# Kernel tuning notes

Hardware: AMD Instinct MI355X
Metric: run time of the kernel (lower is better)

The kernel has to match this reference:

```python
import jax, jax.numpy as jnp
import numpy as np

D_MODEL = 1024
NHEAD = 16
HEAD_DIM = D_MODEL // NHEAD
B, S = 8, 1024
NEG = -1e9  # finite stand-in for -inf (same softmax result, grad-safe)


def setup_inputs() -> dict:
    key = jax.random.key(0)
    ks = jax.random.split(key, 12)
    sc = 1.0 / np.sqrt(D_MODEL)
    inp = {
        "q": jax.random.normal(ks[0], (B, S, D_MODEL), jnp.float32),
        "k": jax.random.normal(ks[1], (B, S, D_MODEL), jnp.float32),
        "v": jax.random.normal(ks[2], (B, S, D_MODEL), jnp.float32),
        "padding_mask": jax.random.bernoulli(ks[3], 0.1, (B, S)),
        "causal_mask": jnp.where(jnp.tril(jnp.ones((S, S), bool)), 0.0, NEG).astype(jnp.float32),
        "wq": jax.random.normal(ks[4], (D_MODEL, D_MODEL), jnp.float32) * sc,
        "bq": jax.random.normal(ks[5], (D_MODEL,), jnp.float32) * sc,
        "wk": jax.random.normal(ks[6], (D_MODEL, D_MODEL), jnp.float32) * sc,
        "wv": jax.random.normal(ks[7], (D_MODEL, D_MODEL), jnp.float32) * sc,
        "bv": jax.random.normal(ks[8], (D_MODEL,), jnp.float32) * sc,
        "wo": jax.random.normal(ks[9], (D_MODEL, D_MODEL), jnp.float32) * sc,
        "bo": jax.random.normal(ks[10], (D_MODEL,), jnp.float32) * sc,
    }
    return inp


def reference(q, k, v, padding_mask, causal_mask, wq, bq, wk, wv, bv, wo, bo):
    b = q.shape[0]
    # projections (torch Linear: x @ W.T + b); k_linear has no bias
    qp = q @ wq.T + bq
    kp = k @ wk.T
    vp = v @ wv.T + bv
    # [B, S, H, Dh] -> [B, H, S, Dh]
    qh = qp.reshape(b, -1, NHEAD, HEAD_DIM).transpose(0, 2, 1, 3)
    kh = kp.reshape(b, -1, NHEAD, HEAD_DIM).transpose(0, 2, 1, 3)
    vh = vp.reshape(b, -1, NHEAD, HEAD_DIM).transpose(0, 2, 1, 3)
    scores = jnp.einsum("bhqd,bhkd->bhqk", qh, kh) / np.sqrt(HEAD_DIM).astype(np.float32)
    scores = jnp.where(padding_mask[:, None, None, :], NEG, scores)
    scores = scores + causal_mask[None, None, :, :]
    attn = jax.nn.softmax(scores, axis=-1)
    out = jnp.einsum("bhqk,bhkd->bhqd", attn, vh)
    out = out.transpose(0, 2, 1, 3).reshape(b, -1, D_MODEL)
    return out @ wo.T + bo
```

## Files before the change

### kernel.cpp

```cpp
#include <hip/hip_runtime.h>
#include <hip/hip_bf16.h>
#include <cstdint>
#include <math.h>


typedef __bf16 bf16_t;
typedef __bf16 bf16x8 __attribute__((ext_vector_type(8)));
typedef __bf16 bf16x4 __attribute__((ext_vector_type(4)));
typedef float  f32x4  __attribute__((ext_vector_type(4)));

#define MFMA16(a, b, c) __builtin_amdgcn_mfma_f32_16x16x32_bf16((a), (b), (c), 0, 0, 0)
#define NEGV (-1e9f)

__device__ __forceinline__ void gl_lds16(const void* gp, void* lp) {
  __builtin_amdgcn_global_load_lds(
      (__attribute__((address_space(1))) void*)(gp),
      (__attribute__((address_space(3))) void*)(lp), 16, 0, 0);
}

__device__ __forceinline__ unsigned int pk2(float lo, float hi) {
  unsigned short a = __builtin_bit_cast(unsigned short, (bf16_t)lo);
  unsigned short b = __builtin_bit_cast(unsigned short, (bf16_t)hi);
  return (unsigned int)a | ((unsigned int)b << 16);
}

__device__ __forceinline__ void cvt_body(const float* __restrict__ in,
                                         bf16_t* __restrict__ out, int i, int n8) {
  if (i < n8) {
    const float4* p = reinterpret_cast<const float4*>(in) + (size_t)i * 2;
    float4 a = p[0], b = p[1];
    bf16x8 r = {(bf16_t)a.x, (bf16_t)a.y, (bf16_t)a.z, (bf16_t)a.w,
                (bf16_t)b.x, (bf16_t)b.y, (bf16_t)b.z, (bf16_t)b.w};
    *reinterpret_cast<bf16x8*>(out + (size_t)i * 8) = r;
  }
}

__global__ __launch_bounds__(256) void cvt_qkv(const float* __restrict__ a, const float* __restrict__ b,
                                               const float* __restrict__ c,
                                               bf16_t* __restrict__ oa, bf16_t* __restrict__ ob,
                                               bf16_t* __restrict__ oc, int n8) {
  const float* in = blockIdx.y == 0 ? a : (blockIdx.y == 1 ? b : c);
  bf16_t* out     = blockIdx.y == 0 ? oa : (blockIdx.y == 1 ? ob : oc);
  cvt_body(in, out, blockIdx.x * 256 + threadIdx.x, n8);
}

__global__ __launch_bounds__(256) void cvt_w4(const float* __restrict__ a, const float* __restrict__ b,
                                              const float* __restrict__ c, const float* __restrict__ d,
                                              bf16_t* __restrict__ oa, bf16_t* __restrict__ ob,
                                              bf16_t* __restrict__ oc, bf16_t* __restrict__ od, int n8) {
  const float* in = blockIdx.y == 0 ? a : (blockIdx.y == 1 ? b : (blockIdx.y == 2 ? c : d));
  bf16_t* out     = blockIdx.y == 0 ? oa : (blockIdx.y == 1 ? ob : (blockIdx.y == 2 ? oc : od));
  cvt_body(in, out, blockIdx.x * 256 + threadIdx.x, n8);
}

__device__ __forceinline__ void panel_decode(int r, int& bx, int& by) {
  const int t8 = r >> 3;
  bx = t8 & 7;
  by = ((t8 >> 3) << 3) | (r & 7);
}

__global__ __launch_bounds__(256) void gemm_qkv(const bf16_t* __restrict__ qbf,
                                                const bf16_t* __restrict__ kbf,
                                                const bf16_t* __restrict__ vbf,
                                                const bf16_t* __restrict__ wqb,
                                                const bf16_t* __restrict__ wkb,
                                                const bf16_t* __restrict__ wvb,
                                                const float* __restrict__ bq,
                                                const float* __restrict__ bv,
                                                bf16_t* __restrict__ qp,
                                                bf16_t* __restrict__ kp,
                                                bf16_t* __restrict__ vtw) {
  __shared__ bf16_t smem[4][128 * 32];
  const int z = blockIdx.y;
  const bf16_t* A = z == 0 ? qbf : (z == 1 ? kbf : vbf);
  const bf16_t* W = z == 0 ? wqb : (z == 1 ? wkb : wvb);
  const int t = threadIdx.x;
  const int w = t >> 6, l = t & 63, lr = l & 15, lg = l >> 4;
  int bx, by;
  panel_decode((int)blockIdx.x, bx, by);
  const int m0 = by * 128, n0 = bx * 128;
  const int wm = (w >> 1) * 64, wn = (w & 1) * 64;
  const int K = 1024, N = 1024;

  f32x4 acc[4][4] = {};
  const bf16_t* Ag = A + (size_t)(m0 + (t >> 2)) * K + (t & 3) * 8;
  const bf16_t* Wg = W + (size_t)(n0 + (t >> 2)) * K + (t & 3) * 8;

  auto stage = [&](int buf, int kt) {
    gl_lds16(Ag + kt,                  (char*)(smem[buf])     + t * 16);
    gl_lds16(Ag + kt + (size_t)64 * K, (char*)(smem[buf])     + 4096 + t * 16);
    gl_lds16(Wg + kt,                  (char*)(smem[2 + buf]) + t * 16);
    gl_lds16(Wg + kt + (size_t)64 * K, (char*)(smem[2 + buf]) + 4096 + t * 16);
  };

  stage(0, 0);
  __syncthreads();

  for (int it = 0; it < 32; ++it) {
    const int cur = it & 1;
    if (it < 31) stage(cur ^ 1, (it + 1) * 32);

    const char* AsB = (const char*)(smem[cur]);
    const char* BsB = (const char*)(smem[2 + cur]);
    bf16x8 af[4], bfr[4];
#pragma unroll
    for (int mt = 0; mt < 4; mt++)
      af[mt] = *reinterpret_cast<const bf16x8*>(AsB + ((wm + mt * 16 + lr) * 32 + lg * 8) * 2);
#pragma unroll
    for (int nt = 0; nt < 4; nt++)
      bfr[nt] = *reinterpret_cast<const bf16x8*>(BsB + ((wn + nt * 16 + lr) * 32 + lg * 8) * 2);
#pragma unroll
    for (int mt = 0; mt < 4; mt++)
#pragma unroll
      for (int nt = 0; nt < 4; nt++)
        acc[mt][nt] = MFMA16(af[mt], bfr[nt], acc[mt][nt]);
    __syncthreads();
  }

  if (z != 2) {
    bf16_t* outp = (z == 0) ? qp : kp;
    const float sc = (z == 0) ? 0.125f : 1.0f;
#pragma unroll
    for (int nt = 0; nt < 4; nt++) {
      const int col = n0 + wn + nt * 16 + lr;
      const float bb = (z == 0) ? bq[col] : 0.0f;
#pragma unroll
      for (int mt = 0; mt < 4; mt++)
#pragma unroll
        for (int i = 0; i < 4; i++) {
          const int row = m0 + wm + mt * 16 + lg * 4 + i;
          outp[(size_t)row * N + col] = (bf16_t)((acc[mt][nt][i] + bb) * sc);
        }
    }
  } else {
    char* T = (char*)smem;
#pragma unroll
    for (int nt = 0; nt < 4; nt++) {
      const int col_l = wn + nt * 16 + lr;
      const float bb = bv[n0 + col_l];
#pragma unroll
      for (int mt = 0; mt < 4; mt++)
#pragma unroll
        for (int i = 0; i < 4; i++) {
          const int row_l = wm + mt * 16 + lg * 4 + i;
          *(bf16_t*)(T + col_l * 256 + ((row_l * 2) ^ ((col_l & 7) << 4))) =
              (bf16_t)(acc[mt][nt][i] + bb);
        }
    }
    __syncthreads();
    const int b = m0 >> 10, s0 = m0 & 1023;
    const int c_l = t >> 1, half = t & 1;
    bf16_t* dst = vtw + (size_t)(b * 1024 + n0 + c_l) * 1024 + s0 + half * 64;
    const char* Trow = T + c_l * 256;
    const int sw = c_l & 7;
#pragma unroll
    for (int jj = 0; jj < 8; jj++) {
      const int lc = half * 8 + jj;
      bf16x8 vv = *reinterpret_cast<const bf16x8*>(Trow + ((lc ^ sw) << 4));
      *reinterpret_cast<bf16x8*>(dst + jj * 8) = vv;
    }
  }
}

__global__ __launch_bounds__(256) void gemm_out(const bf16_t* __restrict__ A,
                                                const bf16_t* __restrict__ W,
                                                const float* __restrict__ bias,
                                                float* __restrict__ outp) {
  __shared__ bf16_t smem[4][128 * 32];
  const int t = threadIdx.x;
  const int w = t >> 6, l = t & 63, lr = l & 15, lg = l >> 4;
  int bx, by;
  panel_decode((int)blockIdx.x, bx, by);
  const int m0 = by * 128, n0 = bx * 128;
  const int wm = (w >> 1) * 64, wn = (w & 1) * 64;
  const int K = 1024, N = 1024;

  f32x4 acc[4][4] = {};
  const bf16_t* Ag = A + (size_t)(m0 + (t >> 2)) * K + (t & 3) * 8;
  const bf16_t* Wg = W + (size_t)(n0 + (t >> 2)) * K + (t & 3) * 8;

  auto stage = [&](int buf, int kt) {
    gl_lds16(Ag + kt,                  (char*)(smem[buf])     + t * 16);
    gl_lds16(Ag + kt + (size_t)64 * K, (char*)(smem[buf])     + 4096 + t * 16);
    gl_lds16(Wg + kt,                  (char*)(smem[2 + buf]) + t * 16);
    gl_lds16(Wg + kt + (size_t)64 * K, (char*)(smem[2 + buf]) + 4096 + t * 16);
  };

  stage(0, 0);
  __syncthreads();

  for (int it = 0; it < 32; ++it) {
    const int cur = it & 1;
    if (it < 31) stage(cur ^ 1, (it + 1) * 32);

    const char* AsB = (const char*)(smem[cur]);
    const char* BsB = (const char*)(smem[2 + cur]);
    bf16x8 af[4], bfr[4];
#pragma unroll
    for (int mt = 0; mt < 4; mt++)
      af[mt] = *reinterpret_cast<const bf16x8*>(AsB + ((wm + mt * 16 + lr) * 32 + lg * 8) * 2);
#pragma unroll
    for (int nt = 0; nt < 4; nt++)
      bfr[nt] = *reinterpret_cast<const bf16x8*>(BsB + ((wn + nt * 16 + lr) * 32 + lg * 8) * 2);
#pragma unroll
    for (int mt = 0; mt < 4; mt++)
#pragma unroll
      for (int nt = 0; nt < 4; nt++)
        acc[mt][nt] = MFMA16(af[mt], bfr[nt], acc[mt][nt]);
    __syncthreads();
  }

#pragma unroll
  for (int nt = 0; nt < 4; nt++) {
    const int col = n0 + wn + nt * 16 + lr;
    const float bb = bias[col];
#pragma unroll
    for (int mt = 0; mt < 4; mt++)
#pragma unroll
      for (int i = 0; i < 4; i++) {
        const int row = m0 + wm + mt * 16 + lg * 4 + i;
        outp[(size_t)row * N + col] = acc[mt][nt][i] + bb;
      }
  }
}

__device__ __forceinline__ void pack_bfly(const f32x4 (&s)[4], int lg,
                                          bf16x8& pbv0, bf16x8& pbv1) {
  unsigned int u[4][2], sh[4][2];
#pragma unroll
  for (int nt = 0; nt < 4; nt++) {
    u[nt][0] = pk2(s[nt][0], s[nt][1]);
    u[nt][1] = pk2(s[nt][2], s[nt][3]);
  }
#pragma unroll
  for (int nt = 0; nt < 4; nt++) {
    sh[nt][0] = (unsigned int)__shfl_xor((int)u[nt][0], 16, 64);
    sh[nt][1] = (unsigned int)__shfl_xor((int)u[nt][1], 16, 64);
  }
  const bool ev = (lg & 1) == 0;
  unsigned int Y[8];
  Y[0] = ev ? u[0][0] : sh[1][0];  Y[1] = ev ? u[0][1] : sh[1][1];
  Y[2] = ev ? u[2][0] : sh[3][0];  Y[3] = ev ? u[2][1] : sh[3][1];
  Y[4] = ev ? sh[0][0] : u[1][0];  Y[5] = ev ? sh[0][1] : u[1][1];
  Y[6] = ev ? sh[2][0] : u[3][0];  Y[7] = ev ? sh[2][1] : u[3][1];
  const bool mid = (lg == 1) || (lg == 2);
#pragma unroll
  for (int j = 0; j < 8; j++) {
    const unsigned int z = (unsigned int)__shfl_xor((int)Y[j], 48, 64);
    Y[j] = mid ? z : Y[j];
  }
  union U8 { unsigned int u[4]; bf16x8 v; };
  U8 p0, p1;
  p0.u[0] = Y[0]; p0.u[1] = Y[1]; p0.u[2] = Y[4]; p0.u[3] = Y[5];
  p1.u[0] = Y[2]; p1.u[1] = Y[3]; p1.u[2] = Y[6]; p1.u[3] = Y[7];
  pbv0 = p0.v;
  pbv1 = p1.v;
}

__global__ __launch_bounds__(512, 8) void attn_fused(const bf16_t* __restrict__ qp,
                                                     const bf16_t* __restrict__ kp,
                                                     const bf16_t* __restrict__ vt,
                                                     const int* __restrict__ pad,
                                                     bf16_t* __restrict__ outp) {
  __shared__ bf16_t Ks[2][64 * 64];
  __shared__ bf16_t Vts[2][64 * 64];
  __shared__ int padI[1024];
  __shared__ int sfl[8], sfh[8];
  const int t = threadIdx.x, w = t >> 6, l = t & 63, lr = l & 15, lg = l >> 4;
  const int L = (int)blockIdx.x;
  const int bh = (L & 7) + ((L >> 6) << 3);
  const int j = (L >> 3) & 7;
  const int b = bh >> 4, h = bh & 15;
  const int lo = j, hi = 15 - j;

  const int srow = t >> 3, sc = t & 7;
  const int gc = sc ^ (srow & 7);
  const bf16_t* kgb = kp + (size_t)(b * 1024 + srow) * 1024 + h * 64 + gc * 8;
  const bf16_t* vgb = vt + (size_t)(bh * 64 + srow) * 1024 + gc * 8;

  auto stage = [&](int bufi, int k0s) {
    gl_lds16(kgb + (size_t)k0s * 1024, (char*)(Ks[bufi]) + t * 16);
    gl_lds16(vgb + k0s,                (char*)(Vts[bufi]) + t * 16);
  };

  bool unl = false, unh = false;
  for (int jj = t; jj <= hi * 64; jj += 512) {
    const bool u = (pad[b * 1024 + jj] == 0);
    unh |= u;
    unl |= (u && (jj <= lo * 64));
  }
  const bool al = __any(unl), ah = __any(unh);
  if (l == 0) { sfl[w] = al ? 1 : 0; sfh[w] = ah ? 1 : 0; }

  stage(0, 0);
  if (t < 256) gl_lds16(pad + b * 1024 + t * 4, (char*)padI + t * 16);

  const int mytile = (w < 4) ? hi : lo;
  const int qrow_l = mytile * 64 + (w & 3) * 16 + lr;
  const int base16 = mytile * 64 + (w & 3) * 16;
  const bf16_t* qg = qp + (size_t)(b * 1024 + qrow_l) * 1024 + h * 64 + lg * 8;
  const bf16x8 qa0 = *reinterpret_cast<const bf16x8*>(qg);
  const bf16x8 qa1 = *reinterpret_cast<const bf16x8*>(qg + 32);

  __syncthreads();
  int ul = 0, uh = 0;
#pragma unroll
  for (int i = 0; i < 8; i++) { ul |= sfl[i]; uh |= sfh[i]; }
  const bool mydeg = (w < 4) ? (uh == 0) : (ul == 0);
  const int ktEnd = (ul == 0) ? 16 : (hi + 1);

  f32x4 o[4] = {};
  float m_ = -INFINITY, ld_ = 0.0f;

  for (int kt = 0; kt < ktEnd; ++kt) {
    const int cur = kt & 1;
    if (kt + 1 < ktEnd) {
      stage(cur ^ 1, (kt + 1) * 64);
      asm volatile("s_waitcnt vmcnt(2)" ::: "memory");
    } else {
      asm volatile("s_waitcnt vmcnt(0)" ::: "memory");
    }
    __builtin_amdgcn_s_barrier();

    if (kt <= mytile || mydeg) {
      const char* Kb = (const char*)(Ks[cur]);
      const char* Vb = (const char*)(Vts[cur]);
      const int k0 = kt * 64;

      f32x4 s[4] = {};
#pragma unroll
      for (int nt = 0; nt < 4; nt++) {
        const int row = nt * 16 + lr;
        const int sw = (row & 7) << 4;
        bf16x8 kb0 = *reinterpret_cast<const bf16x8*>(Kb + row * 128 + ((lg * 16) ^ sw));
        bf16x8 kb1 = *reinterpret_cast<const bf16x8*>(Kb + row * 128 + ((lg * 16 + 64) ^ sw));
        s[nt] = MFMA16(kb0, qa0, s[nt]);
        s[nt] = MFMA16(kb1, qa1, s[nt]);
      }

      const bool nc = (k0 + 63 > base16);
#pragma unroll
      for (int nt = 0; nt < 4; nt++) {
        const int kc4 = k0 + nt * 16 + lg * 4;
        const int4 pd = *reinterpret_cast<const int4*>(&padI[kc4]);
        const int pdv[4] = {pd.x, pd.y, pd.z, pd.w};
#pragma unroll
        for (int i = 0; i < 4; i++) {
          float v = s[nt][i];
          if (pdv[i]) v = NEGV;
          if (nc && (kc4 + i > qrow_l)) v += NEGV;
          s[nt][i] = v;
        }
      }

      float mx = s[0][0];
#pragma unroll
      for (int nt = 0; nt < 4; nt++)
#pragma unroll
        for (int i = 0; i < 4; i++) mx = fmaxf(mx, s[nt][i]);
      mx = fmaxf(mx, __shfl_xor(mx, 16, 64));
      mx = fmaxf(mx, __shfl_xor(mx, 32, 64));

      if (!__all(mx <= m_ - 88.0f)) {
        if (!__all(mx <= m_ + 8.0f)) {
          const float mn = fmaxf(m_, mx);
          const float scl = __expf(m_ - mn);
          m_ = mn;
          ld_ *= scl;
#pragma unroll
          for (int nt = 0; nt < 4; nt++) o[nt] *= scl;
        }
        float a = 0.0f;
#pragma unroll
        for (int nt = 0; nt < 4; nt++)
#pragma unroll
          for (int i = 0; i < 4; i++) {
            const float p = __expf(s[nt][i] - m_);
            s[nt][i] = p;
            a += p;
          }
        a += __shfl_xor(a, 16, 64);
        a += __shfl_xor(a, 32, 64);
        ld_ += a;

        bf16x8 pb0, pb1;
        pack_bfly(s, lg, pb0, pb1);

#pragma unroll
        for (int nt = 0; nt < 4; nt++) {
          const int vrow = nt * 16 + lr;
          const int vsw = (vrow & 7) << 4;
          bf16x8 vf0 = *reinterpret_cast<const bf16x8*>(Vb + vrow * 128 + ((lg * 16) ^ vsw));
          bf16x8 vf1 = *reinterpret_cast<const bf16x8*>(Vb + vrow * 128 + ((64 + lg * 16) ^ vsw));
          o[nt] = MFMA16(vf0, pb0, o[nt]);
          o[nt] = MFMA16(vf1, pb1, o[nt]);
        }
      }
    }
    __builtin_amdgcn_s_barrier();
  }

  const float rinv = 1.0f / ld_;
#pragma unroll
  for (int nt = 0; nt < 4; nt++) {
    bf16x4 r = {(bf16_t)(o[nt][0] * rinv), (bf16_t)(o[nt][1] * rinv),
                (bf16_t)(o[nt][2] * rinv), (bf16_t)(o[nt][3] * rinv)};
    *reinterpret_cast<bf16x4*>(outp + (size_t)(b * 1024 + qrow_l) * 1024 + h * 64 + nt * 16 + lg * 4) = r;
  }
}

extern "C" void kernel_launch(void* const* d_in, const int* in_sizes, int n_in,
                              void* d_out, int out_size, void* d_ws, size_t ws_size,
                              hipStream_t stream) {
  const float* q   = (const float*)d_in[0];
  const float* k   = (const float*)d_in[1];
  const float* v   = (const float*)d_in[2];
  const int*   pad = (const int*)d_in[3];
  const float* wq  = (const float*)d_in[5];
  const float* bq  = (const float*)d_in[6];
  const float* wk  = (const float*)d_in[7];
  const float* wv  = (const float*)d_in[8];
  const float* bv  = (const float*)d_in[9];
  const float* wo  = (const float*)d_in[10];
  const float* bo  = (const float*)d_in[11];

  const int M = 8192, N = 1024;
  const int nBig = M * N;
  const int nW   = N * 1024;

  char* ws = (char*)d_ws;
  const size_t MiB = 1024 * 1024;
  bf16_t* qbf = (bf16_t*)(ws + 0 * MiB);
  bf16_t* kbf = (bf16_t*)(ws + 16 * MiB);
  bf16_t* vbf = (bf16_t*)(ws + 32 * MiB);
  bf16_t* qp  = (bf16_t*)(ws + 48 * MiB);
  bf16_t* kp  = (bf16_t*)(ws + 64 * MiB);
  bf16_t* vtw = (bf16_t*)(ws + 80 * MiB);
  bf16_t* wqb = (bf16_t*)(ws + 96 * MiB);
  bf16_t* wkb = (bf16_t*)(ws + 98 * MiB);
  bf16_t* wvb = (bf16_t*)(ws + 100 * MiB);
  bf16_t* wob = (bf16_t*)(ws + 102 * MiB);
  bf16_t* attnO = qbf;

  cvt_qkv<<<dim3(nBig / 2048, 3), 256, 0, stream>>>(q, k, v, qbf, kbf, vbf, nBig / 8);
  cvt_w4 <<<dim3(nW / 2048, 4), 256, 0, stream>>>(wq, wk, wv, wo, wqb, wkb, wvb, wob, nW / 8);

  gemm_qkv<<<dim3(512, 3), 256, 0, stream>>>(qbf, kbf, vbf, wqb, wkb, wvb, bq, bv, qp, kp, vtw);

  attn_fused<<<1024, 512, 0, stream>>>(qp, kp, vtw, pad, attnO);

  gemm_out<<<512, 256, 0, stream>>>(attnO, wob, bo, (float*)d_out);
}
```

Baseline: 189.8 us.

## Fuse fp32-to-bf16 activation conversion into QKV projection GEMM A-tile loads

```diff
diff --git a/kernel.cpp b/kernel.cpp
--- a/kernel.cpp
+++ b/kernel.cpp
@@ -35,15 +35,6 @@
   }
 }
 
-__global__ __launch_bounds__(256) void cvt_qkv(const float* __restrict__ a, const float* __restrict__ b,
-                                               const float* __restrict__ c,
-                                               bf16_t* __restrict__ oa, bf16_t* __restrict__ ob,
-                                               bf16_t* __restrict__ oc, int n8) {
-  const float* in = blockIdx.y == 0 ? a : (blockIdx.y == 1 ? b : c);
-  bf16_t* out     = blockIdx.y == 0 ? oa : (blockIdx.y == 1 ? ob : oc);
-  cvt_body(in, out, blockIdx.x * 256 + threadIdx.x, n8);
-}
-
 __global__ __launch_bounds__(256) void cvt_w4(const float* __restrict__ a, const float* __restrict__ b,
                                               const float* __restrict__ c, const float* __restrict__ d,
                                               bf16_t* __restrict__ oa, bf16_t* __restrict__ ob,
@@ -59,9 +50,9 @@
   by = ((t8 >> 3) << 3) | (r & 7);
 }
 
-__global__ __launch_bounds__(256) void gemm_qkv(const bf16_t* __restrict__ qbf,
-                                                const bf16_t* __restrict__ kbf,
-                                                const bf16_t* __restrict__ vbf,
+__global__ __launch_bounds__(256) void gemm_qkv(const float* __restrict__ qf,
+                                                const float* __restrict__ kf,
+                                                const float* __restrict__ vf,
                                                 const bf16_t* __restrict__ wqb,
                                                 const bf16_t* __restrict__ wkb,
                                                 const bf16_t* __restrict__ wvb,
@@ -72,7 +63,7 @@
                                                 bf16_t* __restrict__ vtw) {
   __shared__ bf16_t smem[4][128 * 32];
   const int z = blockIdx.y;
-  const bf16_t* A = z == 0 ? qbf : (z == 1 ? kbf : vbf);
+  const float*  A = z == 0 ? qf : (z == 1 ? kf : vf);
   const bf16_t* W = z == 0 ? wqb : (z == 1 ? wkb : wvb);
   const int t = threadIdx.x;
   const int w = t >> 6, l = t & 63, lr = l & 15, lg = l >> 4;
@@ -83,23 +74,43 @@
   const int K = 1024, N = 1024;
 
   f32x4 acc[4][4] = {};
-  const bf16_t* Ag = A + (size_t)(m0 + (t >> 2)) * K + (t & 3) * 8;
+
+  const int arow = t >> 1, acol = (t & 1) * 16;
+  const float* Agf = A + (size_t)(m0 + arow) * K + acol;
+  char* adst0 = (char*)(smem[0]) + arow * 64 + (t & 1) * 32;
+  char* adst1 = (char*)(smem[1]) + arow * 64 + (t & 1) * 32;
   const bf16_t* Wg = W + (size_t)(n0 + (t >> 2)) * K + (t & 3) * 8;
 
-  auto stage = [&](int buf, int kt) {
-    gl_lds16(Ag + kt,                  (char*)(smem[buf])     + t * 16);
-    gl_lds16(Ag + kt + (size_t)64 * K, (char*)(smem[buf])     + 4096 + t * 16);
+  float4 a0, a1, a2, a3;
+  auto loadA = [&](int kt) {
+    const float4* p = reinterpret_cast<const float4*>(Agf + kt);
+    a0 = p[0]; a1 = p[1]; a2 = p[2]; a3 = p[3];
+  };
+  auto writeA = [&](int buf) {
+    bf16x8 r0 = {(bf16_t)a0.x, (bf16_t)a0.y, (bf16_t)a0.z, (bf16_t)a0.w,
+                 (bf16_t)a1.x, (bf16_t)a1.y, (bf16_t)a1.z, (bf16_t)a1.w};
+    bf16x8 r1 = {(bf16_t)a2.x, (bf16_t)a2.y, (bf16_t)a2.z, (bf16_t)a2.w,
+                 (bf16_t)a3.x, (bf16_t)a3.y, (bf16_t)a3.z, (bf16_t)a3.w};
+    char* d = buf ? adst1 : adst0;
+    *reinterpret_cast<bf16x8*>(d) = r0;
+    *reinterpret_cast<bf16x8*>(d + 16) = r1;
+  };
+  auto stageB = [&](int buf, int kt) {
     gl_lds16(Wg + kt,                  (char*)(smem[2 + buf]) + t * 16);
     gl_lds16(Wg + kt + (size_t)64 * K, (char*)(smem[2 + buf]) + 4096 + t * 16);
   };
 
-  stage(0, 0);
+  loadA(0);
+  stageB(0, 0);
+  writeA(0);
   __syncthreads();
 
   for (int it = 0; it < 32; ++it) {
     const int cur = it & 1;
-    if (it < 31) stage(cur ^ 1, (it + 1) * 32);
-
+    if (it < 31) {
+      loadA((it + 1) * 32);
+      stageB(cur ^ 1, (it + 1) * 32);
+    }
     const char* AsB = (const char*)(smem[cur]);
     const char* BsB = (const char*)(smem[2 + cur]);
     bf16x8 af[4], bfr[4];
@@ -114,6 +125,7 @@
 #pragma unroll
       for (int nt = 0; nt < 4; nt++)
         acc[mt][nt] = MFMA16(af[mt], bfr[nt], acc[mt][nt]);
+    if (it < 31) writeA(cur ^ 1);
     __syncthreads();
   }
 
@@ -424,15 +436,11 @@
   const float* wo  = (const float*)d_in[10];
   const float* bo  = (const float*)d_in[11];
 
-  const int M = 8192, N = 1024;
-  const int nBig = M * N;
-  const int nW   = N * 1024;
+  const int nW = 1024 * 1024;
 
   char* ws = (char*)d_ws;
   const size_t MiB = 1024 * 1024;
-  bf16_t* qbf = (bf16_t*)(ws + 0 * MiB);
-  bf16_t* kbf = (bf16_t*)(ws + 16 * MiB);
-  bf16_t* vbf = (bf16_t*)(ws + 32 * MiB);
+  bf16_t* attnO = (bf16_t*)(ws + 0 * MiB);
   bf16_t* qp  = (bf16_t*)(ws + 48 * MiB);
   bf16_t* kp  = (bf16_t*)(ws + 64 * MiB);
   bf16_t* vtw = (bf16_t*)(ws + 80 * MiB);
@@ -440,12 +448,10 @@
   bf16_t* wkb = (bf16_t*)(ws + 98 * MiB);
   bf16_t* wvb = (bf16_t*)(ws + 100 * MiB);
   bf16_t* wob = (bf16_t*)(ws + 102 * MiB);
-  bf16_t* attnO = qbf;
-
-  cvt_qkv<<<dim3(nBig / 2048, 3), 256, 0, stream>>>(q, k, v, qbf, kbf, vbf, nBig / 8);
-  cvt_w4 <<<dim3(nW / 2048, 4), 256, 0, stream>>>(wq, wk, wv, wo, wqb, wkb, wvb, wob, nW / 8);
-
-  gemm_qkv<<<dim3(512, 3), 256, 0, stream>>>(qbf, kbf, vbf, wqb, wkb, wvb, bq, bv, qp, kp, vtw);
+
+  cvt_w4<<<dim3(nW / 2048, 4), 256, 0, stream>>>(wq, wk, wv, wo, wqb, wkb, wvb, wob, nW / 8);
+
+  gemm_qkv<<<dim3(512, 3), 256, 0, stream>>>(q, k, v, wqb, wkb, wvb, bq, bv, qp, kp, vtw);
 
   attn_fused<<<1024, 512, 0, stream>>>(qp, kp, vtw, pad, attnO);
 
```

After: 194.4 us. 1.02x slower.

## Triple-buffer GEMM LDS staging with swizzled layout and merge conversion kernels

Applied to the files above, without the earlier changes.

```diff
diff --git a/kernel.cpp b/kernel.cpp
--- a/kernel.cpp
+++ b/kernel.cpp
@@ -25,32 +25,34 @@
 }
 
 __device__ __forceinline__ void cvt_body(const float* __restrict__ in,
-                                         bf16_t* __restrict__ out, int i, int n8) {
-  if (i < n8) {
-    const float4* p = reinterpret_cast<const float4*>(in) + (size_t)i * 2;
-    float4 a = p[0], b = p[1];
-    bf16x8 r = {(bf16_t)a.x, (bf16_t)a.y, (bf16_t)a.z, (bf16_t)a.w,
-                (bf16_t)b.x, (bf16_t)b.y, (bf16_t)b.z, (bf16_t)b.w};
-    *reinterpret_cast<bf16x8*>(out + (size_t)i * 8) = r;
-  }
-}
-
-__global__ __launch_bounds__(256) void cvt_qkv(const float* __restrict__ a, const float* __restrict__ b,
-                                               const float* __restrict__ c,
-                                               bf16_t* __restrict__ oa, bf16_t* __restrict__ ob,
-                                               bf16_t* __restrict__ oc, int n8) {
-  const float* in = blockIdx.y == 0 ? a : (blockIdx.y == 1 ? b : c);
-  bf16_t* out     = blockIdx.y == 0 ? oa : (blockIdx.y == 1 ? ob : oc);
-  cvt_body(in, out, blockIdx.x * 256 + threadIdx.x, n8);
-}
-
-__global__ __launch_bounds__(256) void cvt_w4(const float* __restrict__ a, const float* __restrict__ b,
-                                              const float* __restrict__ c, const float* __restrict__ d,
-                                              bf16_t* __restrict__ oa, bf16_t* __restrict__ ob,
-                                              bf16_t* __restrict__ oc, bf16_t* __restrict__ od, int n8) {
-  const float* in = blockIdx.y == 0 ? a : (blockIdx.y == 1 ? b : (blockIdx.y == 2 ? c : d));
-  bf16_t* out     = blockIdx.y == 0 ? oa : (blockIdx.y == 1 ? ob : (blockIdx.y == 2 ? oc : od));
-  cvt_body(in, out, blockIdx.x * 256 + threadIdx.x, n8);
+                                         bf16_t* __restrict__ out, int i) {
+  const float4* p = reinterpret_cast<const float4*>(in) + (size_t)i * 2;
+  float4 a = p[0], b = p[1];
+  bf16x8 r = {(bf16_t)a.x, (bf16_t)a.y, (bf16_t)a.z, (bf16_t)a.w,
+              (bf16_t)b.x, (bf16_t)b.y, (bf16_t)b.z, (bf16_t)b.w};
+  *reinterpret_cast<bf16x8*>(out + (size_t)i * 8) = r;
+}
+
+__global__ __launch_bounds__(256) void cvt_all(
+    const float* __restrict__ q, const float* __restrict__ k, const float* __restrict__ v,
+    const float* __restrict__ wq, const float* __restrict__ wk,
+    const float* __restrict__ wv, const float* __restrict__ wo,
+    bf16_t* __restrict__ oq, bf16_t* __restrict__ ok, bf16_t* __restrict__ ov,
+    bf16_t* __restrict__ owq, bf16_t* __restrict__ owk,
+    bf16_t* __restrict__ owv, bf16_t* __restrict__ owo) {
+  const int bid = (int)blockIdx.x;
+  if (bid < 12288) {
+    const int s = bid >> 12;
+    const int i = (bid & 4095) * 256 + (int)threadIdx.x;
+    cvt_body(s == 0 ? q : (s == 1 ? k : v),
+             s == 0 ? oq : (s == 1 ? ok : ov), i);
+  } else {
+    const int r = bid - 12288;
+    const int s = r >> 9;
+    const int i = (r & 511) * 256 + (int)threadIdx.x;
+    cvt_body(s == 0 ? wq : (s == 1 ? wk : (s == 2 ? wv : wo)),
+             s == 0 ? owq : (s == 1 ? owk : (s == 2 ? owv : owo)), i);
+  }
 }
 
 __device__ __forceinline__ void panel_decode(int r, int& bx, int& by) {
@@ -70,7 +72,7 @@
                                                 bf16_t* __restrict__ qp,
                                                 bf16_t* __restrict__ kp,
                                                 bf16_t* __restrict__ vtw) {
-  __shared__ bf16_t smem[4][128 * 32];
+  __shared__ bf16_t smem[6][128 * 32];
   const int z = blockIdx.y;
   const bf16_t* A = z == 0 ? qbf : (z == 1 ? kbf : vbf);
   const bf16_t* W = z == 0 ? wqb : (z == 1 ? wkb : wvb);
@@ -83,38 +85,42 @@
   const int K = 1024, N = 1024;
 
   f32x4 acc[4][4] = {};
-  const bf16_t* Ag = A + (size_t)(m0 + (t >> 2)) * K + (t & 3) * 8;
-  const bf16_t* Wg = W + (size_t)(n0 + (t >> 2)) * K + (t & 3) * 8;
-
-  auto stage = [&](int buf, int kt) {
+  const int swsrc = ((t & 3) ^ ((t >> 3) & 3)) * 8;
+  const bf16_t* Ag = A + (size_t)(m0 + (t >> 2)) * K + swsrc;
+  const bf16_t* Wg = W + (size_t)(n0 + (t >> 2)) * K + swsrc;
+
+  auto stage = [&](int buf, int tile) {
+    const int kt = tile * 32;
     gl_lds16(Ag + kt,                  (char*)(smem[buf])     + t * 16);
     gl_lds16(Ag + kt + (size_t)64 * K, (char*)(smem[buf])     + 4096 + t * 16);
-    gl_lds16(Wg + kt,                  (char*)(smem[2 + buf]) + t * 16);
-    gl_lds16(Wg + kt + (size_t)64 * K, (char*)(smem[2 + buf]) + 4096 + t * 16);
+    gl_lds16(Wg + kt,                  (char*)(smem[3 + buf]) + t * 16);
+    gl_lds16(Wg + kt + (size_t)64 * K, (char*)(smem[3 + buf]) + 4096 + t * 16);
   };
 
   stage(0, 0);
-  __syncthreads();
-
+  stage(1, 1);
+
+  const int cofs = ((lg ^ ((lr >> 1) & 3)) << 4);
   for (int it = 0; it < 32; ++it) {
-    const int cur = it & 1;
-    if (it < 31) stage(cur ^ 1, (it + 1) * 32);
-
-    const char* AsB = (const char*)(smem[cur]);
-    const char* BsB = (const char*)(smem[2 + cur]);
+    if (it < 31) asm volatile("s_waitcnt vmcnt(4)" ::: "memory");
+    else         asm volatile("s_waitcnt vmcnt(0)" ::: "memory");
+    __builtin_amdgcn_s_barrier();
+    if (it + 2 < 32) stage((it + 2) % 3, it + 2);
+
+    const char* AsB = (const char*)(smem[it % 3]);
+    const char* BsB = (const char*)(smem[3 + it % 3]);
     bf16x8 af[4], bfr[4];
 #pragma unroll
     for (int mt = 0; mt < 4; mt++)
-      af[mt] = *reinterpret_cast<const bf16x8*>(AsB + ((wm + mt * 16 + lr) * 32 + lg * 8) * 2);
+      af[mt] = *reinterpret_cast<const bf16x8*>(AsB + (wm + mt * 16 + lr) * 64 + cofs);
 #pragma unroll
     for (int nt = 0; nt < 4; nt++)
-      bfr[nt] = *reinterpret_cast<const bf16x8*>(BsB + ((wn + nt * 16 + lr) * 32 + lg * 8) * 2);
+      bfr[nt] = *reinterpret_cast<const bf16x8*>(BsB + (wn + nt * 16 + lr) * 64 + cofs);
 #pragma unroll
     for (int mt = 0; mt < 4; mt++)
 #pragma unroll
       for (int nt = 0; nt < 4; nt++)
         acc[mt][nt] = MFMA16(af[mt], bfr[nt], acc[mt][nt]);
-    __syncthreads();
   }
 
   if (z != 2) {
@@ -133,6 +139,7 @@
         }
     }
   } else {
+    __syncthreads();
     char* T = (char*)smem;
 #pragma unroll
     for (int nt = 0; nt < 4; nt++) {
@@ -166,7 +173,7 @@
                                                 const bf16_t* __restrict__ W,
                                                 const float* __restrict__ bias,
                                                 float* __restrict__ outp) {
-  __shared__ bf16_t smem[4][128 * 32];
+  __shared__ bf16_t smem[6][128 * 32];
   const int t = threadIdx.x;
   const int w = t >> 6, l = t & 63, lr = l & 15, lg = l >> 4;
   int bx, by;
@@ -176,38 +183,42 @@
   const int K = 1024, N = 1024;
 
   f32x4 acc[4][4] = {};
-  const bf16_t* Ag = A + (size_t)(m0 + (t >> 2)) * K + (t & 3) * 8;
-  const bf16_t* Wg = W + (size_t)(n0 + (t >> 2)) * K + (t & 3) * 8;
-
-  auto stage = [&](int buf, int kt) {
+  const int swsrc = ((t & 3) ^ ((t >> 3) & 3)) * 8;
+  const bf16_t* Ag = A + (size_t)(m0 + (t >> 2)) * K + swsrc;
+  const bf16_t* Wg = W + (size_t)(n0 + (t >> 2)) * K + swsrc;
+
+  auto stage = [&](int buf, int tile) {
+    const int kt = tile * 32;
     gl_lds16(Ag + kt,                  (char*)(smem[buf])     + t * 16);
     gl_lds16(Ag + kt + (size_t)64 * K, (char*)(smem[buf])     + 4096 + t * 16);
-    gl_lds16(Wg + kt,                  (char*)(smem[2 + buf]) + t * 16);
-    gl_lds16(Wg + kt + (size_t)64 * K, (char*)(smem[2 + buf]) + 4096 + t * 16);
+    gl_lds16(Wg + kt,                  (char*)(smem[3 + buf]) + t * 16);
+    gl_lds16(Wg + kt + (size_t)64 * K, (char*)(smem[3 + buf]) + 4096 + t * 16);
   };
 
   stage(0, 0);
-  __syncthreads();
-
+  stage(1, 1);
+
+  const int cofs = ((lg ^ ((lr >> 1) & 3)) << 4);
   for (int it = 0; it < 32; ++it) {
-    const int cur = it & 1;
-    if (it < 31) stage(cur ^ 1, (it + 1) * 32);
-
-    const char* AsB = (const char*)(smem[cur]);
-    const char* BsB = (const char*)(smem[2 + cur]);
+    if (it < 31) asm volatile("s_waitcnt vmcnt(4)" ::: "memory");
+    else         asm volatile("s_waitcnt vmcnt(0)" ::: "memory");
+    __builtin_amdgcn_s_barrier();
+    if (it + 2 < 32) stage((it + 2) % 3, it + 2);
+
+    const char* AsB = (const char*)(smem[it % 3]);
+    const char* BsB = (const char*)(smem[3 + it % 3]);
     bf16x8 af[4], bfr[4];
 #pragma unroll
     for (int mt = 0; mt < 4; mt++)
-      af[mt] = *reinterpret_cast<const bf16x8*>(AsB + ((wm + mt * 16 + lr) * 32 + lg * 8) * 2);
+      af[mt] = *reinterpret_cast<const bf16x8*>(AsB + (wm + mt * 16 + lr) * 64 + cofs);
 #pragma unroll
     for (int nt = 0; nt < 4; nt++)
-      bfr[nt] = *reinterpret_cast<const bf16x8*>(BsB + ((wn + nt * 16 + lr) * 32 + lg * 8) * 2);
+      bfr[nt] = *reinterpret_cast<const bf16x8*>(BsB + (wn + nt * 16 + lr) * 64 + cofs);
 #pragma unroll
     for (int mt = 0; mt < 4; mt++)
 #pragma unroll
       for (int nt = 0; nt < 4; nt++)
         acc[mt][nt] = MFMA16(af[mt], bfr[nt], acc[mt][nt]);
-    __syncthreads();
   }
 
 #pragma unroll
@@ -424,10 +435,6 @@
   const float* wo  = (const float*)d_in[10];
   const float* bo  = (const float*)d_in[11];
 
-  const int M = 8192, N = 1024;
-  const int nBig = M * N;
-  const int nW   = N * 1024;
-
   char* ws = (char*)d_ws;
   const size_t MiB = 1024 * 1024;
   bf16_t* qbf = (bf16_t*)(ws + 0 * MiB);
@@ -442,8 +449,8 @@
   bf16_t* wob = (bf16_t*)(ws + 102 * MiB);
   bf16_t* attnO = qbf;
 
-  cvt_qkv<<<dim3(nBig / 2048, 3), 256, 0, stream>>>(q, k, v, qbf, kbf, vbf, nBig / 8);
-  cvt_w4 <<<dim3(nW / 2048, 4), 256, 0, stream>>>(wq, wk, wv, wo, wqb, wkb, wvb, wob, nW / 8);
+  cvt_all<<<14336, 256, 0, stream>>>(q, k, v, wq, wk, wv, wo,
+                                     qbf, kbf, vbf, wqb, wkb, wvb, wob);
 
   gemm_qkv<<<dim3(512, 3), 256, 0, stream>>>(qbf, kbf, vbf, wqb, wkb, wvb, bq, bv, qp, kp, vtw);
 
```

Result: no change. 187.4 us (-1.3%).
